# Optimization experiments

Hardware: AMD Instinct MI355X
Metric: run time of the kernel (lower is better)

The kernel has to match this reference:

```python
import jax, jax.numpy as jnp
import numpy as np

N_NODES = 100000
IN_F = 256
OUT_F = 128
N_EDGES = 1600000


def setup_inputs() -> dict:
    key = jax.random.key(0)
    k1, k2, k3, k4 = jax.random.split(key, 4)
    inputs = jax.random.normal(k1, (N_NODES, IN_F), dtype=jnp.float32)
    edge = jax.random.randint(k2, (2, N_EDGES), 0, N_NODES, dtype=jnp.int64)
    # xavier_uniform for weight [in, out]
    bw = float(np.sqrt(6.0 / (IN_F + OUT_F)))
    weight = jax.random.uniform(k3, (IN_F, OUT_F), minval=-bw, maxval=bw, dtype=jnp.float32)
    ba = float(np.sqrt(6.0 / (OUT_F + 1)))
    a = jax.random.uniform(k4, (OUT_F, 1), minval=-ba, maxval=ba, dtype=jnp.float32)
    return {"inputs": inputs, "edge": edge, "weight": weight, "a": a}


def reference(inputs, edge, weight, a):
    # h: [N, out_features]
    h = inputs @ weight
    # edge-wise gather + abs-diff: [E, out_features]
    diff = jnp.abs(h[edge[0]] - h[edge[1]])
    # dot with attention vector a, relu, squeeze -> [E]
    edge_weight = jax.nn.relu((diff @ a).squeeze(-1))
    return (h, edge_weight)
```

## Files before the change

### kernel.cpp

```cpp
#include <hip/hip_runtime.h>
#include <hip/hip_bf16.h>
#include <stdint.h>

typedef __bf16 bf16x8 __attribute__((ext_vector_type(8)));
typedef float  f32x4  __attribute__((ext_vector_type(4)));

#define M_NODES 100000
#define K_IN    256
#define N_OUT   128
#define N_EDGE  1600000

template <bool FULL>
__device__ __forceinline__ void gemm_tile(
    const float* __restrict__ in, float* __restrict__ h,
    __hip_bfloat16* __restrict__ hmir,
    const bf16x8 (&bfrag)[8][2], const int m0, const int lr, const int q,
    const int nb)
{
    f32x4 acc[4][2];
    #pragma unroll
    for (int mt = 0; mt < 4; ++mt)
        #pragma unroll
        for (int nt = 0; nt < 2; ++nt)
            acc[mt][nt] = f32x4{0.f, 0.f, 0.f, 0.f};

    #pragma unroll
    for (int k8 = 0; k8 < 8; ++k8) {
        const int ka = k8 * 32 + q * 8;
        bf16x8 afrag[4];
        #pragma unroll
        for (int mt = 0; mt < 4; ++mt) {
            const int row = m0 + mt * 16 + lr;
            if (FULL || row < M_NODES) {
                const float* ap = in + (size_t)row * K_IN + ka;
                const f32x4 a0 = *(const f32x4*)ap;
                const f32x4 a1 = *(const f32x4*)(ap + 4);
                #pragma unroll
                for (int j = 0; j < 4; ++j) {
                    afrag[mt][j]     = (__bf16)a0[j];
                    afrag[mt][4 + j] = (__bf16)a1[j];
                }
            } else {
                #pragma unroll
                for (int j = 0; j < 8; ++j) afrag[mt][j] = (__bf16)0.f;
            }
        }
        #pragma unroll
        for (int mt = 0; mt < 4; ++mt)
            #pragma unroll
            for (int nt = 0; nt < 2; ++nt)
                acc[mt][nt] = __builtin_amdgcn_mfma_f32_16x16x32_bf16(
                    afrag[mt], bfrag[k8][nt], acc[mt][nt], 0, 0, 0);
    }

    #pragma unroll
    for (int mt = 0; mt < 4; ++mt) {
        const int rb = m0 + mt * 16 + q * 4;
        if (!FULL && rb >= M_NODES) continue;
        #pragma unroll
        for (int nt = 0; nt < 2; ++nt) {
            const int col = nb + nt * 16 + lr;
            #pragma unroll
            for (int r = 0; r < 4; ++r) {
                const float v = acc[mt][nt][r];
                __builtin_nontemporal_store(v, h + (size_t)(rb + r) * N_OUT + col);
                hmir[(size_t)(rb + r) * N_OUT + col] = __float2bfloat16(v);
            }
        }
    }
}

__global__ __launch_bounds__(256) void gemm_h_mfma(
    const float* __restrict__ in,
    const float* __restrict__ w,
    float* __restrict__ h,
    __hip_bfloat16* __restrict__ hmir)
{
    const int lane = threadIdx.x & 63;
    const int wave = threadIdx.x >> 6;
    const int nb   = wave * 32;
    const int lr   = lane & 15;
    const int q    = lane >> 4;

    bf16x8 bfrag[8][2];
    #pragma unroll
    for (int k8 = 0; k8 < 8; ++k8) {
        const int ka = k8 * 32 + q * 8;
        #pragma unroll
        for (int nt = 0; nt < 2; ++nt) {
            const int col = nb + nt * 16 + lr;
            #pragma unroll
            for (int j = 0; j < 8; ++j)
                bfrag[k8][nt][j] = (__bf16)w[(size_t)(ka + j) * N_OUT + col];
        }
    }

    const int ntiles = (M_NODES + 63) / 64;
    const int nfull  = M_NODES / 64;
    for (int t = blockIdx.x; t < ntiles; t += gridDim.x) {
        const int m0 = t * 64;
        if (t < nfull) gemm_tile<true >(in, h, hmir, bfrag, m0, lr, q, nb);
        else           gemm_tile<false>(in, h, hmir, bfrag, m0, lr, q, nb);
    }
}

__device__ inline int detect_i64(const uint32_t* p) {
    return __popcll(__ballot(p[2 * (threadIdx.x & 63) + 1] == 0u)) >= 60;
}

__global__ __launch_bounds__(256) void edge_kernel_bf16(
    const __hip_bfloat16* __restrict__ hm,
    const uint32_t* __restrict__ edge_raw,
    const float* __restrict__ a,
    float* __restrict__ ew,
    int E)
{
    const int e64 = detect_i64(edge_raw);
    const int s  = threadIdx.x & 15;
    const int g  = (int)((blockIdx.x * 256 + threadIdx.x) >> 4);
    const int e0 = g * 4;
    if (e0 >= E) return;

    const __bf16* hb = (const __bf16*)hm;
    const f32x4 a0 = *(const f32x4*)(a + s * 8);
    const f32x4 a1 = *(const f32x4*)(a + s * 8 + 4);

    if (e0 + 3 < E) {
        int srcs[4], dsts[4];
        if (e64) {
            const uint4 s01 = *(const uint4*)(edge_raw + 2 * (size_t)e0);
            const uint4 s23 = *(const uint4*)(edge_raw + 2 * (size_t)e0 + 4);
            const uint4 d01 = *(const uint4*)(edge_raw + 2 * ((size_t)E + e0));
            const uint4 d23 = *(const uint4*)(edge_raw + 2 * ((size_t)E + e0) + 4);
            srcs[0] = (int)s01.x; srcs[1] = (int)s01.z;
            srcs[2] = (int)s23.x; srcs[3] = (int)s23.z;
            dsts[0] = (int)d01.x; dsts[1] = (int)d01.z;
            dsts[2] = (int)d23.x; dsts[3] = (int)d23.z;
        } else {
            const int4 sv = *(const int4*)((const int*)edge_raw + e0);
            const int4 dv = *(const int4*)((const int*)edge_raw + (size_t)E + e0);
            srcs[0] = sv.x; srcs[1] = sv.y; srcs[2] = sv.z; srcs[3] = sv.w;
            dsts[0] = dv.x; dsts[1] = dv.y; dsts[2] = dv.z; dsts[3] = dv.w;
        }

        bf16x8 hs[4], hd[4];
        #pragma unroll
        for (int u = 0; u < 4; ++u) {
            hs[u] = *(const bf16x8*)(hb + (size_t)srcs[u] * N_OUT + s * 8);
            hd[u] = *(const bf16x8*)(hb + (size_t)dsts[u] * N_OUT + s * 8);
        }

        f32x4 r;
        #pragma unroll
        for (int u = 0; u < 4; ++u) {
            float sum = 0.f;
            #pragma unroll
            for (int i = 0; i < 4; ++i)
                sum += fabsf((float)hs[u][i] - (float)hd[u][i]) * a0[i];
            #pragma unroll
            for (int i = 0; i < 4; ++i)
                sum += fabsf((float)hs[u][4 + i] - (float)hd[u][4 + i]) * a1[i];
            sum += __shfl_xor(sum, 1, 64);
            sum += __shfl_xor(sum, 2, 64);
            sum += __shfl_xor(sum, 4, 64);
            sum += __shfl_xor(sum, 8, 64);
            r[u] = fmaxf(sum, 0.f);
        }
        if (s == 0) *(f32x4*)(ew + e0) = r;
    } else {
        for (int e = e0; e < E; ++e) {
            int src, dst;
            if (e64) {
                src = (int)edge_raw[2 * (size_t)e];
                dst = (int)edge_raw[2 * ((size_t)E + e)];
            } else {
                const int* e32 = (const int*)edge_raw;
                src = e32[e];
                dst = e32[(size_t)E + e];
            }
            const bf16x8 hs = *(const bf16x8*)(hb + (size_t)src * N_OUT + s * 8);
            const bf16x8 hd = *(const bf16x8*)(hb + (size_t)dst * N_OUT + s * 8);
            float sum = 0.f;
            #pragma unroll
            for (int i = 0; i < 4; ++i)
                sum += fabsf((float)hs[i] - (float)hd[i]) * a0[i];
            #pragma unroll
            for (int i = 0; i < 4; ++i)
                sum += fabsf((float)hs[4 + i] - (float)hd[4 + i]) * a1[i];
            sum += __shfl_xor(sum, 1, 64);
            sum += __shfl_xor(sum, 2, 64);
            sum += __shfl_xor(sum, 4, 64);
            sum += __shfl_xor(sum, 8, 64);
            if (s == 0) ew[e] = fmaxf(sum, 0.f);
        }
    }
}

__global__ __launch_bounds__(256) void edge_kernel_f32(
    const float* __restrict__ h,
    const uint32_t* __restrict__ edge_raw,
    const float* __restrict__ a,
    float* __restrict__ ew,
    int E)
{
    const int e64 = detect_i64(edge_raw);
    const int s = threadIdx.x & 15;
    const int e = (int)((blockIdx.x * 256 + threadIdx.x) >> 4);
    if (e >= E) return;

    int src, dst;
    if (e64) {
        src = (int)edge_raw[2 * (size_t)e];
        dst = (int)edge_raw[2 * ((size_t)E + e)];
    } else {
        const int* e32 = (const int*)edge_raw;
        src = e32[e];
        dst = e32[(size_t)E + e];
    }

    const f32x4 s0 = *(const f32x4*)(h + (size_t)src * N_OUT + s * 8);
    const f32x4 s1 = *(const f32x4*)(h + (size_t)src * N_OUT + s * 8 + 4);
    const f32x4 d0 = *(const f32x4*)(h + (size_t)dst * N_OUT + s * 8);
    const f32x4 d1 = *(const f32x4*)(h + (size_t)dst * N_OUT + s * 8 + 4);
    const f32x4 a0 = *(const f32x4*)(a + s * 8);
    const f32x4 a1 = *(const f32x4*)(a + s * 8 + 4);

    float sum = 0.f;
    #pragma unroll
    for (int i = 0; i < 4; ++i) sum += fabsf(s0[i] - d0[i]) * a0[i];
    #pragma unroll
    for (int i = 0; i < 4; ++i) sum += fabsf(s1[i] - d1[i]) * a1[i];

    sum += __shfl_xor(sum, 1, 64);
    sum += __shfl_xor(sum, 2, 64);
    sum += __shfl_xor(sum, 4, 64);
    sum += __shfl_xor(sum, 8, 64);

    if (s == 0) ew[e] = fmaxf(sum, 0.f);
}

extern "C" void kernel_launch(void* const* d_in, const int* in_sizes, int n_in,
                              void* d_out, int out_size, void* d_ws, size_t ws_size,
                              hipStream_t stream) {
    const float*    in   = (const float*)d_in[0];
    const uint32_t* edge = (const uint32_t*)d_in[1];
    const float*    w    = (const float*)d_in[2];
    const float*    a    = (const float*)d_in[3];

    float* h  = (float*)d_out;
    float* ew = h + (size_t)M_NODES * N_OUT;

    const size_t mirror_bytes = (size_t)M_NODES * N_OUT * sizeof(__hip_bfloat16);
    __hip_bfloat16* hmir =
        (ws_size >= mirror_bytes) ? (__hip_bfloat16*)d_ws : nullptr;

    if (hmir) {
        gemm_h_mfma<<<dim3(512), dim3(256), 0, stream>>>(in, w, h, hmir);
        const int egroups = (N_EDGE + 3) / 4;
        const int eblocks = (egroups * 16 + 255) / 256;
        edge_kernel_bf16<<<dim3(eblocks), dim3(256), 0, stream>>>(
            hmir, edge, a, ew, N_EDGE);
    } else {
        gemm_h_mfma<<<dim3(512), dim3(256), 0, stream>>>(
            in, w, h, (__hip_bfloat16*)d_ws);
        const int eblocks = (N_EDGE * 16 + 255) / 256;
        edge_kernel_f32<<<dim3(eblocks), dim3(256), 0, stream>>>(
            h, edge, a, ew, N_EDGE);
    }
}
```

Baseline: 298.6 us.

## Bucket edges by source-node XCD range so each XCD's L2 holds its gather rows

Adds a histogram, prefix and scatter pass that groups edges by which eighth of the node range their source falls in, packing src, dst and edge id into 64-bit records. A new edge kernel maps block index modulo 8 to a bucket, so blocks on the same XCD gather source rows from a single 12.5k-node slice of the bf16 mirror. This targets the poor L2 locality of random row gathers across the eight XCD L2 caches. In exchange it adds three extra launches plus a memset and extra edge traffic (read twice, 12.8 MB of records written and read back), and it assumes the round-robin block-to-XCD mapping. Destination rows remain random.

```diff
diff --git a/kernel.cpp b/kernel.cpp
--- a/kernel.cpp
+++ b/kernel.cpp
@@ -4,11 +4,17 @@
 
 typedef __bf16 bf16x8 __attribute__((ext_vector_type(8)));
 typedef float  f32x4  __attribute__((ext_vector_type(4)));
+typedef uint32_t u32x4 __attribute__((ext_vector_type(4)));
+typedef unsigned long long u64;
 
 #define M_NODES 100000
 #define K_IN    256
 #define N_OUT   128
 #define N_EDGE  1600000
+
+#define NXCD          8
+#define NODES_PER_XCD 12500
+#define SCATTER_CH    2048
 
 template <bool FULL>
 __device__ __forceinline__ void gemm_tile(
@@ -106,6 +112,139 @@
 
 __device__ inline int detect_i64(const uint32_t* p) {
     return __popcll(__ballot(p[2 * (threadIdx.x & 63) + 1] == 0u)) >= 60;
+}
+
+__global__ __launch_bounds__(256) void edge_hist(
+    const uint32_t* __restrict__ edge_raw, int E, uint32_t* __restrict__ hist)
+{
+    __shared__ uint32_t lh[NXCD];
+    if (threadIdx.x < NXCD) lh[threadIdx.x] = 0;
+    const int e64 = detect_i64(edge_raw);
+    __syncthreads();
+    const int stride = gridDim.x * 256;
+    for (int e = blockIdx.x * 256 + threadIdx.x; e < E; e += stride) {
+        const int src = e64 ? (int)edge_raw[2 * (size_t)e]
+                            : ((const int*)edge_raw)[e];
+        atomicAdd(&lh[src / NODES_PER_XCD], 1u);
+    }
+    __syncthreads();
+    if (threadIdx.x < NXCD) atomicAdd(&hist[threadIdx.x], lh[threadIdx.x]);
+}
+
+__global__ void bucket_prefix(uint32_t* __restrict__ ctrl)
+{
+    if (threadIdx.x == 0) {
+        uint32_t s = 0;
+        for (int b = 0; b < NXCD; ++b) {
+            ctrl[8 + b]  = s;
+            ctrl[16 + b] = s;
+            s += ctrl[b];
+        }
+    }
+}
+
+__global__ __launch_bounds__(256) void edge_scatter(
+    const uint32_t* __restrict__ edge_raw, int E,
+    uint32_t* __restrict__ cursor,
+    u64* __restrict__ rec)
+{
+    const int e64 = detect_i64(edge_raw);
+    __shared__ uint32_t cnt[NXCD], base[NXCD], cur[NXCD];
+    if (threadIdx.x < NXCD) { cnt[threadIdx.x] = 0; cur[threadIdx.x] = 0; }
+    __syncthreads();
+
+    const int e0 = blockIdx.x * SCATTER_CH;
+    int src[8], dst[8], bb[8];
+    #pragma unroll
+    for (int u = 0; u < 8; ++u) {
+        const int e = e0 + u * 256 + threadIdx.x;
+        if (e < E) {
+            if (e64) {
+                src[u] = (int)edge_raw[2 * (size_t)e];
+                dst[u] = (int)edge_raw[2 * ((size_t)E + e)];
+            } else {
+                src[u] = ((const int*)edge_raw)[e];
+                dst[u] = ((const int*)edge_raw)[(size_t)E + e];
+            }
+            bb[u] = src[u] / NODES_PER_XCD;
+            atomicAdd(&cnt[bb[u]], 1u);
+        } else bb[u] = -1;
+    }
+    __syncthreads();
+    if (threadIdx.x < NXCD)
+        base[threadIdx.x] = atomicAdd(&cursor[threadIdx.x], cnt[threadIdx.x]);
+    __syncthreads();
+    #pragma unroll
+    for (int u = 0; u < 8; ++u) {
+        if (bb[u] >= 0) {
+            const int e = e0 + u * 256 + threadIdx.x;
+            const uint32_t pos = base[bb[u]] + atomicAdd(&cur[bb[u]], 1u);
+            const u64 r = (u64)(uint32_t)src[u] | ((u64)(uint32_t)dst[u] << 17)
+                        | ((u64)(uint32_t)e << 34);
+            __builtin_nontemporal_store(r, rec + pos);
+        }
+    }
+}
+
+__global__ __launch_bounds__(256) void edge_compute_sorted(
+    const __hip_bfloat16* __restrict__ hm,
+    const u64* __restrict__ rec,
+    const uint32_t* __restrict__ ctrl,
+    const float* __restrict__ a,
+    float* __restrict__ ew)
+{
+    const int s   = threadIdx.x & 15;
+    const int grp = threadIdx.x >> 4;
+    const int b   = blockIdx.x & 7;
+    const int j   = blockIdx.x >> 3;
+    const uint32_t BPB = gridDim.x >> 3;
+    const uint32_t n   = ctrl[b];
+    const uint32_t st  = ctrl[8 + b];
+
+    const __bf16* hb = (const __bf16*)hm;
+    const f32x4 a0 = *(const f32x4*)(a + s * 8);
+    const f32x4 a1 = *(const f32x4*)(a + s * 8 + 4);
+
+    for (uint32_t base = (uint32_t)j * 64 + (uint32_t)grp * 4; base < n;
+         base += BPB * 64) {
+        const uint32_t rem = n - base;
+        const int nv = rem < 4u ? (int)rem : 4;
+
+        u64 r[4];
+        #pragma unroll
+        for (int u = 0; u < 4; ++u)
+            r[u] = (u < nv) ? __builtin_nontemporal_load(rec + st + base + u)
+                            : 0ull;
+
+        bf16x8 hs[4], hd[4];
+        #pragma unroll
+        for (int u = 0; u < 4; ++u) {
+            const int src = (int)(r[u] & 0x1FFFF);
+            const int dst = (int)((r[u] >> 17) & 0x1FFFF);
+            hs[u] = *(const bf16x8*)(hb + (size_t)src * N_OUT + s * 8);
+            const u32x4 dv = __builtin_nontemporal_load(
+                (const u32x4*)(hb + (size_t)dst * N_OUT + s * 8));
+            hd[u] = __builtin_bit_cast(bf16x8, dv);
+        }
+
+        #pragma unroll
+        for (int u = 0; u < 4; ++u) {
+            float sum = 0.f;
+            #pragma unroll
+            for (int i = 0; i < 4; ++i)
+                sum += fabsf((float)hs[u][i] - (float)hd[u][i]) * a0[i];
+            #pragma unroll
+            for (int i = 0; i < 4; ++i)
+                sum += fabsf((float)hs[u][4 + i] - (float)hd[u][4 + i]) * a1[i];
+            sum += __shfl_xor(sum, 1, 64);
+            sum += __shfl_xor(sum, 2, 64);
+            sum += __shfl_xor(sum, 4, 64);
+            sum += __shfl_xor(sum, 8, 64);
+            if (s == 0 && u < nv)
+                __builtin_nontemporal_store(fmaxf(sum, 0.f),
+                                            ew + (uint32_t)(r[u] >> 34));
+        }
+    }
 }
 
 __global__ __launch_bounds__(256) void edge_kernel_bf16(
@@ -150,7 +289,7 @@
             hd[u] = *(const bf16x8*)(hb + (size_t)dsts[u] * N_OUT + s * 8);
         }
 
-        f32x4 r;
+        f32x4 rr;
         #pragma unroll
         for (int u = 0; u < 4; ++u) {
             float sum = 0.f;
@@ -164,9 +303,9 @@
             sum += __shfl_xor(sum, 2, 64);
             sum += __shfl_xor(sum, 4, 64);
             sum += __shfl_xor(sum, 8, 64);
-            r[u] = fmaxf(sum, 0.f);
-        }
-        if (s == 0) *(f32x4*)(ew + e0) = r;
+            rr[u] = fmaxf(sum, 0.f);
+        }
+        if (s == 0) *(f32x4*)(ew + e0) = rr;
     } else {
         for (int e = e0; e < E; ++e) {
             int src, dst;
@@ -251,10 +390,25 @@
     float* ew = h + (size_t)M_NODES * N_OUT;
 
     const size_t mirror_bytes = (size_t)M_NODES * N_OUT * sizeof(__hip_bfloat16);
-    __hip_bfloat16* hmir =
-        (ws_size >= mirror_bytes) ? (__hip_bfloat16*)d_ws : nullptr;
-
-    if (hmir) {
+    const size_t ctrl_off     = mirror_bytes;
+    const size_t rec_off      = ctrl_off + 1024;
+    const size_t sorted_bytes = rec_off + (size_t)N_EDGE * sizeof(u64);
+
+    __hip_bfloat16* hmir = (ws_size >= mirror_bytes) ? (__hip_bfloat16*)d_ws : nullptr;
+
+    if (hmir && ws_size >= sorted_bytes) {
+        uint32_t* ctrl = (uint32_t*)((char*)d_ws + ctrl_off);
+        u64*      rec  = (u64*)((char*)d_ws + rec_off);
+
+        hipMemsetAsync(ctrl, 0, 1024, stream);
+        edge_hist<<<dim3(512), dim3(256), 0, stream>>>(edge, N_EDGE, ctrl);
+        bucket_prefix<<<dim3(1), dim3(64), 0, stream>>>(ctrl);
+        edge_scatter<<<dim3((N_EDGE + SCATTER_CH - 1) / SCATTER_CH), dim3(256),
+                       0, stream>>>(edge, N_EDGE, ctrl + 16, rec);
+        gemm_h_mfma<<<dim3(512), dim3(256), 0, stream>>>(in, w, h, hmir);
+        edge_compute_sorted<<<dim3(25000), dim3(256), 0, stream>>>(
+            hmir, rec, ctrl, a, ew);
+    } else if (hmir) {
         gemm_h_mfma<<<dim3(512), dim3(256), 0, stream>>>(in, w, h, hmir);
         const int egroups = (N_EDGE + 3) / 4;
         const int eblocks = (egroups * 16 + 255) / 256;
```

After: 379.7 us. 27.2% more time.

## Launch one GEMM tile per block, prefetch A, reload W fragments per half

Applied to the files above, without the earlier changes.

The GEMM kernel drops the persistent 512-block grid-stride loop and launches one block per 64-row tile. The weight fragments are no longer held in registers for the whole kernel; each block loads them in two halves. The A loads are software-pipelined by one k-step so global loads overlap the MFMA work, and launch bounds now request 3 blocks per SM to raise occupancy. In exchange, every block re-reads and re-converts W (which comes from L2), so redundant W traffic and conversion work grows.

```diff
diff --git a/kernel.cpp b/kernel.cpp
--- a/kernel.cpp
+++ b/kernel.cpp
@@ -12,10 +12,9 @@
 
 template <bool FULL>
 __device__ __forceinline__ void gemm_tile(
-    const float* __restrict__ in, float* __restrict__ h,
-    __hip_bfloat16* __restrict__ hmir,
-    const bf16x8 (&bfrag)[8][2], const int m0, const int lr, const int q,
-    const int nb)
+    const float* __restrict__ in, const float* __restrict__ w,
+    float* __restrict__ h, __hip_bfloat16* __restrict__ hmir,
+    const int m0, const int lr, const int q, const int nb)
 {
     f32x4 acc[4][2];
     #pragma unroll
@@ -24,33 +23,67 @@
         for (int nt = 0; nt < 2; ++nt)
             acc[mt][nt] = f32x4{0.f, 0.f, 0.f, 0.f};
 
-    #pragma unroll
-    for (int k8 = 0; k8 < 8; ++k8) {
+    auto loadA = [&](int k8, f32x4 (&A0)[4], f32x4 (&A1)[4]) {
         const int ka = k8 * 32 + q * 8;
-        bf16x8 afrag[4];
         #pragma unroll
         for (int mt = 0; mt < 4; ++mt) {
             const int row = m0 + mt * 16 + lr;
             if (FULL || row < M_NODES) {
                 const float* ap = in + (size_t)row * K_IN + ka;
-                const f32x4 a0 = *(const f32x4*)ap;
-                const f32x4 a1 = *(const f32x4*)(ap + 4);
+                A0[mt] = *(const f32x4*)ap;
+                A1[mt] = *(const f32x4*)(ap + 4);
+            } else {
+                A0[mt] = f32x4{0.f, 0.f, 0.f, 0.f};
+                A1[mt] = f32x4{0.f, 0.f, 0.f, 0.f};
+            }
+        }
+    };
+
+    f32x4 ca[4], cb[4];
+    loadA(0, ca, cb);
+
+    #pragma unroll
+    for (int half = 0; half < 2; ++half) {
+        bf16x8 bfrag[4][2];
+        #pragma unroll
+        for (int k4 = 0; k4 < 4; ++k4) {
+            const int ka = (half * 4 + k4) * 32 + q * 8;
+            #pragma unroll
+            for (int nt = 0; nt < 2; ++nt) {
+                const int col = nb + nt * 16 + lr;
+                #pragma unroll
+                for (int j = 0; j < 8; ++j)
+                    bfrag[k4][nt][j] = (__bf16)w[(size_t)(ka + j) * N_OUT + col];
+            }
+        }
+
+        #pragma unroll
+        for (int k4 = 0; k4 < 4; ++k4) {
+            f32x4 na[4], nb_[4];
+            const int k8 = half * 4 + k4;
+            if (k8 < 7) loadA(k8 + 1, na, nb_);
+
+            bf16x8 af[4];
+            #pragma unroll
+            for (int mt = 0; mt < 4; ++mt)
                 #pragma unroll
                 for (int j = 0; j < 4; ++j) {
-                    afrag[mt][j]     = (__bf16)a0[j];
-                    afrag[mt][4 + j] = (__bf16)a1[j];
+                    af[mt][j]     = (__bf16)ca[mt][j];
+                    af[mt][4 + j] = (__bf16)cb[mt][j];
                 }
-            } else {
-                #pragma unroll
-                for (int j = 0; j < 8; ++j) afrag[mt][j] = (__bf16)0.f;
-            }
-        }
-        #pragma unroll
-        for (int mt = 0; mt < 4; ++mt)
-            #pragma unroll
-            for (int nt = 0; nt < 2; ++nt)
-                acc[mt][nt] = __builtin_amdgcn_mfma_f32_16x16x32_bf16(
-                    afrag[mt], bfrag[k8][nt], acc[mt][nt], 0, 0, 0);
+
+            #pragma unroll
+            for (int mt = 0; mt < 4; ++mt)
+                #pragma unroll
+                for (int nt = 0; nt < 2; ++nt)
+                    acc[mt][nt] = __builtin_amdgcn_mfma_f32_16x16x32_bf16(
+                        af[mt], bfrag[k4][nt], acc[mt][nt], 0, 0, 0);
+
+            if (k8 < 7) {
+                #pragma unroll
+                for (int mt = 0; mt < 4; ++mt) { ca[mt] = na[mt]; cb[mt] = nb_[mt]; }
+            }
+        }
     }
 
     #pragma unroll
@@ -70,7 +103,7 @@
     }
 }
 
-__global__ __launch_bounds__(256) void gemm_h_mfma(
+__global__ __launch_bounds__(256, 3) void gemm_h_mfma(
     const float* __restrict__ in,
     const float* __restrict__ w,
     float* __restrict__ h,
@@ -82,26 +115,11 @@
     const int lr   = lane & 15;
     const int q    = lane >> 4;
 
-    bf16x8 bfrag[8][2];
-    #pragma unroll
-    for (int k8 = 0; k8 < 8; ++k8) {
-        const int ka = k8 * 32 + q * 8;
-        #pragma unroll
-        for (int nt = 0; nt < 2; ++nt) {
-            const int col = nb + nt * 16 + lr;
-            #pragma unroll
-            for (int j = 0; j < 8; ++j)
-                bfrag[k8][nt][j] = (__bf16)w[(size_t)(ka + j) * N_OUT + col];
-        }
-    }
-
-    const int ntiles = (M_NODES + 63) / 64;
-    const int nfull  = M_NODES / 64;
-    for (int t = blockIdx.x; t < ntiles; t += gridDim.x) {
-        const int m0 = t * 64;
-        if (t < nfull) gemm_tile<true >(in, h, hmir, bfrag, m0, lr, q, nb);
-        else           gemm_tile<false>(in, h, hmir, bfrag, m0, lr, q, nb);
-    }
+    const int m0 = blockIdx.x * 64;
+    if (m0 + 64 <= M_NODES)
+        gemm_tile<true >(in, w, h, hmir, m0, lr, q, nb);
+    else
+        gemm_tile<false>(in, w, h, hmir, m0, lr, q, nb);
 }
 
 __device__ inline int detect_i64(const uint32_t* p) {
@@ -150,7 +168,7 @@
             hd[u] = *(const bf16x8*)(hb + (size_t)dsts[u] * N_OUT + s * 8);
         }
 
-        f32x4 r;
+        f32x4 rr;
         #pragma unroll
         for (int u = 0; u < 4; ++u) {
             float sum = 0.f;
@@ -164,9 +182,9 @@
             sum += __shfl_xor(sum, 2, 64);
             sum += __shfl_xor(sum, 4, 64);
             sum += __shfl_xor(sum, 8, 64);
-            r[u] = fmaxf(sum, 0.f);
-        }
-        if (s == 0) *(f32x4*)(ew + e0) = r;
+            rr[u] = fmaxf(sum, 0.f);
+        }
+        if (s == 0) *(f32x4*)(ew + e0) = rr;
     } else {
         for (int e = e0; e < E; ++e) {
             int src, dst;
@@ -254,14 +272,16 @@
     __hip_bfloat16* hmir =
         (ws_size >= mirror_bytes) ? (__hip_bfloat16*)d_ws : nullptr;
 
+    const int gblocks = (M_NODES + 63) / 64;
+
     if (hmir) {
-        gemm_h_mfma<<<dim3(512), dim3(256), 0, stream>>>(in, w, h, hmir);
+        gemm_h_mfma<<<dim3(gblocks), dim3(256), 0, stream>>>(in, w, h, hmir);
         const int egroups = (N_EDGE + 3) / 4;
         const int eblocks = (egroups * 16 + 255) / 256;
         edge_kernel_bf16<<<dim3(eblocks), dim3(256), 0, stream>>>(
             hmir, edge, a, ew, N_EDGE);
     } else {
-        gemm_h_mfma<<<dim3(512), dim3(256), 0, stream>>>(
+        gemm_h_mfma<<<dim3(gblocks), dim3(256), 0, stream>>>(
             in, w, h, (__hip_bfloat16*)d_ws);
         const int eblocks = (N_EDGE * 16 + 255) / 256;
         edge_kernel_f32<<<dim3(eblocks), dim3(256), 0, stream>>>(
```

New measurement: 315.5 us. 5.7% more time.
